# Kernel optimization log

Measured on AMD Instinct MI355X. Metric: run time of the kernel, lower is better.

## Reference

```python
import jax, jax.numpy as jnp
import numpy as np
from jax import lax

B, S, D = 1, 2048, 1280
H = 16
HD = D // H  # 80
L = 2
I = 5120
SCALE = HD ** -0.5
EPS = 1e-6
GH, GW = 64, 32  # patch grid: GH*GW == S
THETA = 10000.0


def _make_rope(dtype=jnp.float32):
    # 2D vision RoPE: half the rotary dims encode row position, half column.
    half = HD // 2  # 40
    inv_freq = 1.0 / (THETA ** (jnp.arange(0, half, 2, dtype=jnp.float32) / half))  # [20]
    hpos = jnp.repeat(jnp.arange(GH, dtype=jnp.float32), GW)  # [S]
    wpos = jnp.tile(jnp.arange(GW, dtype=jnp.float32), GH)    # [S]
    freqs = jnp.concatenate([hpos[:, None] * inv_freq, wpos[:, None] * inv_freq], axis=-1)  # [S, 40]
    emb = jnp.concatenate([freqs, freqs], axis=-1)  # [S, 80]
    return jnp.cos(emb).astype(dtype), jnp.sin(emb).astype(dtype)


def setup_inputs() -> dict:
    key = jax.random.key(0)
    ks = jax.random.split(key, 8)
    cos, sin = _make_rope()
    std = 0.02
    return {
        "hidden_states": jax.random.normal(ks[0], (B, S, D), jnp.float32),
        "cos": cos,
        "sin": sin,
        "qkv_w": jax.random.normal(ks[1], (L, D, 3 * D), jnp.float32) * std,
        "qkv_b": jnp.zeros((L, 3 * D), jnp.float32),
        "proj_w": jax.random.normal(ks[2], (L, D, D), jnp.float32) * std,
        "proj_b": jnp.zeros((L, D), jnp.float32),
        "ln1_g": jnp.ones((L, D), jnp.float32),
        "ln1_b": jnp.zeros((L, D), jnp.float32),
        "ln2_g": jnp.ones((L, D), jnp.float32),
        "ln2_b": jnp.zeros((L, D), jnp.float32),
        "fc1_w": jax.random.normal(ks[3], (L, D, I), jnp.float32) * std,
        "fc1_b": jnp.zeros((L, I), jnp.float32),
        "fc2_w": jax.random.normal(ks[4], (L, I, D), jnp.float32) * std,
        "fc2_b": jnp.zeros((L, D), jnp.float32),
    }


def _layernorm(x, g, b):
    m = jnp.mean(x, axis=-1, keepdims=True)
    v = jnp.mean(jnp.square(x - m), axis=-1, keepdims=True)
    return (x - m) * lax.rsqrt(v + EPS) * g + b


def _rotate_half(x):
    h = x.shape[-1] // 2
    return jnp.concatenate([-x[..., h:], x[..., :h]], axis=-1)


def _block(x, cos, sin, p):
    (qkv_w, qkv_b, proj_w, proj_b, g1, b1, g2, b2, f1w, f1b, f2w, f2b) = p
    # --- attention ---
    h = _layernorm(x, g1, b1)
    qkv = h @ qkv_w + qkv_b                                    # [B,S,3D]
    qkv = qkv.reshape(B, S, 3, H, HD).transpose(2, 0, 3, 1, 4)  # [3,B,H,S,hd]
    q, k, v = qkv[0], qkv[1], qkv[2]
    q = q * cos + _rotate_half(q) * sin                        # cos/sin broadcast over B,H
    k = k * cos + _rotate_half(k) * sin
    scores = jnp.einsum("bhqd,bhkd->bhqk", q, k) * SCALE       # [B,H,S,S]
    w = jax.nn.softmax(scores.astype(jnp.float32), axis=-1).astype(x.dtype)
    o = jnp.einsum("bhqk,bhkd->bhqd", w, v)
    o = o.transpose(0, 2, 1, 3).reshape(B, S, D)
    x = x + (o @ proj_w + proj_b)
    # --- MLP ---
    h = _layernorm(x, g2, b2)
    x = x + jax.nn.gelu(h @ f1w + f1b, approximate=False) @ f2w + f2b
    return x


def reference(hidden_states, cos, sin, qkv_w, qkv_b, proj_w, proj_b,
              ln1_g, ln1_b, ln2_g, ln2_b, fc1_w, fc1_b, fc2_w, fc2_b):
    params = (qkv_w, qkv_b, proj_w, proj_b, ln1_g, ln1_b,
              ln2_g, ln2_b, fc1_w, fc1_b, fc2_w, fc2_b)

    def step(x, p):
        return _block(x, cos, sin, p), None

    out, _ = lax.scan(step, hidden_states, params)
    return out
```

## Files before the change

kernel.cpp:

```cpp
#include <hip/hip_runtime.h>
#include <hip/hip_bf16.h>

using bf16 = __hip_bfloat16;
using short8 = __attribute__((ext_vector_type(8))) short;
using f32x4  = __attribute__((ext_vector_type(4))) float;

#define GLDS16(g, l) __builtin_amdgcn_global_load_lds( \
    (const __attribute__((address_space(1))) void*)(g), \
    (__attribute__((address_space(3))) void*)(l), 16, 0, 0)

constexpr int S  = 2048;
constexpr int D  = 1280;
constexpr int H  = 16;
constexpr int HD = 80;
constexpr int IM = 5120;

__global__ __launch_bounds__(256) void transpose_w(const float* __restrict__ W,
                                                   bf16* __restrict__ Wt,
                                                   int K, int N) {
  __shared__ float t[32][33];
  int tx = threadIdx.x & 31, ty = threadIdx.x >> 5;
  int n0 = blockIdx.x * 32, k0 = blockIdx.y * 32;
#pragma unroll
  for (int i = 0; i < 4; i++)
    t[ty + i * 8][tx] = W[(size_t)(k0 + ty + i * 8) * N + n0 + tx];
  __syncthreads();
#pragma unroll
  for (int i = 0; i < 4; i++)
    Wt[(size_t)(n0 + ty + i * 8) * K + k0 + tx] = __float2bfloat16(t[tx][ty + i * 8]);
}

__global__ __launch_bounds__(256) void transpose_v(const bf16* __restrict__ v,
                                                   bf16* __restrict__ vt) {
  __shared__ bf16 t[16][17];
  int tx = threadIdx.x & 15, ty = threadIdx.x >> 4;
  int s0 = blockIdx.x * 16, d0 = blockIdx.y * 16, h = blockIdx.z;
  t[ty][tx] = v[(size_t)(h * S + s0 + ty) * HD + d0 + tx];
  __syncthreads();
  vt[(size_t)(h * HD + d0 + ty) * S + s0 + tx] = t[tx][ty];
}

__global__ __launch_bounds__(256) void layernorm_k(const float* __restrict__ x,
                                                   const float* __restrict__ g,
                                                   const float* __restrict__ b,
                                                   bf16* __restrict__ h) {
  int row = blockIdx.x, tid = threadIdx.x;
  const float* xr = x + (size_t)row * D;
  float v[5], s1 = 0.f, s2 = 0.f;
#pragma unroll
  for (int i = 0; i < 5; i++) {
    v[i] = xr[tid + i * 256];
    s1 += v[i]; s2 += v[i] * v[i];
  }
#pragma unroll
  for (int o = 32; o > 0; o >>= 1) {
    s1 += __shfl_down(s1, o);
    s2 += __shfl_down(s2, o);
  }
  __shared__ float r1[4], r2[4];
  if ((tid & 63) == 0) { r1[tid >> 6] = s1; r2[tid >> 6] = s2; }
  __syncthreads();
  s1 = r1[0] + r1[1] + r1[2] + r1[3];
  s2 = r2[0] + r2[1] + r2[2] + r2[3];
  float mean = s1 * (1.f / D);
  float rstd = rsqrtf(s2 * (1.f / D) - mean * mean + 1e-6f);
  bf16* hr = h + (size_t)row * D;
#pragma unroll
  for (int i = 0; i < 5; i++) {
    int c = tid + i * 256;
    hr[c] = __float2bfloat16((v[i] - mean) * rstd * g[c] + b[c]);
  }
}

__global__ __launch_bounds__(256) void rope_k(bf16* __restrict__ q, bf16* __restrict__ k,
                                              const float* __restrict__ cs,
                                              const float* __restrict__ sn) {
  int idx = blockIdx.x * 256 + threadIdx.x;
  int p  = idx % 40;
  int t  = idx / 40;
  int s  = t & (S - 1);
  int t2 = t >> 11;
  int hh = t2 & (H - 1);
  bf16* base = ((t2 >> 4) ? k : q) + (size_t)(hh * S + s) * HD;
  float c0 = cs[s * HD + p],      s0 = sn[s * HD + p];
  float c1 = cs[s * HD + p + 40], s1 = sn[s * HD + p + 40];
  float x0 = __bfloat162float(base[p]);
  float x1 = __bfloat162float(base[p + 40]);
  base[p]      = __float2bfloat16(x0 * c0 - x1 * s0);
  base[p + 40] = __float2bfloat16(x1 * c1 + x0 * s1);
}

template <int EPI, int N, int K>
__global__ __launch_bounds__(256, 2) void gemm_bt(const bf16* __restrict__ A,
                                                  const bf16* __restrict__ Bt,
                                                  const float* __restrict__ bias,
                                                  float* __restrict__ X,
                                                  bf16* __restrict__ O) {
  __shared__ __align__(16) short As[128 * 32];
  __shared__ __align__(16) short Bs[128 * 32];
  int tid = threadIdx.x, lane = tid & 63, wid = tid >> 6;
  int l15 = lane & 15, l4 = lane >> 4;
  int wr = wid >> 1, wc = wid & 1;
  int rowBase = blockIdx.y * 128, colBase = blockIdx.x * 128;
  const bf16* Ab = A  + (size_t)rowBase * K;
  const bf16* Bb = Bt + (size_t)colBase * K;

  f32x4 acc[4][4] = {};

  for (int kt = 0; kt < K / 32; kt++) {
#pragma unroll
    for (int i = 0; i < 2; i++) {
      int cb = wid * 128 + i * 64;
      int c  = cb + lane;
      GLDS16(Ab + (c >> 2) * K + kt * 32 + (c & 3) * 8, As + cb * 8);
      GLDS16(Bb + (c >> 2) * K + kt * 32 + (c & 3) * 8, Bs + cb * 8);
    }
    __syncthreads();
    short8 af[4], bfv[4];
    const short8* Av = (const short8*)As;
    const short8* Bv = (const short8*)Bs;
#pragma unroll
    for (int i = 0; i < 4; i++) {
      af[i]  = Av[(wr * 64 + i * 16 + l15) * 4 + l4];
      bfv[i] = Bv[(wc * 64 + i * 16 + l15) * 4 + l4];
    }
#pragma unroll
    for (int m = 0; m < 4; m++)
#pragma unroll
      for (int n = 0; n < 4; n++)
        acc[m][n] = __builtin_amdgcn_mfma_f32_16x16x32_bf16(af[m], bfv[n], acc[m][n], 0, 0, 0);
    __syncthreads();
  }

#pragma unroll
  for (int m = 0; m < 4; m++) {
#pragma unroll
    for (int n = 0; n < 4; n++) {
      int col = colBase + wc * 64 + n * 16 + l15;
      float bs = bias[col];
      int row0 = rowBase + wr * 64 + m * 16 + l4 * 4;
#pragma unroll
      for (int j = 0; j < 4; j++) {
        float val = acc[m][n][j] + bs;
        int row = row0 + j;
        if (EPI == 0) {
          int which = col / D;
          int r2 = col - which * D;
          int hh = r2 / HD, d = r2 - hh * HD;
          O[(size_t)((which * H + hh) * S + row) * HD + d] = __float2bfloat16(val);
        } else if (EPI == 1) {
          X[(size_t)row * N + col] += val;
        } else {
          float gl = 0.5f * val * (1.0f + erff(val * 0.70710678118654752f));
          O[(size_t)row * N + col] = __float2bfloat16(gl);
        }
      }
    }
  }
}

__global__ __launch_bounds__(256) void flash_k(const bf16* __restrict__ q,
                                               const bf16* __restrict__ k,
                                               const bf16* __restrict__ vt,
                                               bf16* __restrict__ o) {
  __shared__ __align__(16) bf16 Qs[128 * 80];
  __shared__ __align__(16) bf16 Ks[64 * 80];
  __shared__ __align__(16) bf16 Vts[80 * 64];
  __shared__ __align__(16) bf16 Ps[128 * 72];
  const float scale = 0.11180339887498949f;
  int tid = threadIdx.x, lane = tid & 63, wid = tid >> 6;
  int l15 = lane & 15, l4 = lane >> 4;
  int hh = blockIdx.y, qb = blockIdx.x * 128;

  const bf16* qg = q + (size_t)(hh * S + qb) * HD;
#pragma unroll
  for (int i = 0; i < 5; i++) {
    int cb = i * 256 + wid * 64;
    GLDS16(qg + (size_t)(cb + lane) * 8, Qs + cb * 8);
  }

  f32x4 oacc[2][5] = {};
  float mst[2][4], lst[2][4];
#pragma unroll
  for (int m = 0; m < 2; m++)
#pragma unroll
    for (int j = 0; j < 4; j++) { mst[m][j] = -3.0e38f; lst[m][j] = 0.f; }

  const short8 zero8 = {0, 0, 0, 0, 0, 0, 0, 0};
  __syncthreads();

  for (int kt = 0; kt < S / 64; kt++) {
    const bf16* kg = k + (size_t)(hh * S + kt * 64) * HD;
    const bf16* vg = vt + (size_t)hh * HD * S + kt * 64;
#pragma unroll
    for (int i = 0; i < 2; i++) {
      int cb = i * 256 + wid * 64;
      int c  = cb + lane;
      GLDS16(kg + c * 8, Ks + cb * 8);
      int hd = c >> 3, cc = (c & 7) ^ (hd & 7);
      GLDS16(vg + hd * S + cc * 8, Vts + cb * 8);
    }
    if (wid < 2) {
      int cb = 512 + wid * 64;
      int c  = cb + lane;
      GLDS16(kg + c * 8, Ks + cb * 8);
      int hd = c >> 3, cc = (c & 7) ^ (hd & 7);
      GLDS16(vg + hd * S + cc * 8, Vts + cb * 8);
    }
    __syncthreads();

    f32x4 sacc[2][4] = {};
#pragma unroll
    for (int kf = 0; kf < 3; kf++) {
      bool act = (kf < 2) || (l4 < 2);
      short8 aq[2], bk[4];
#pragma unroll
      for (int m = 0; m < 2; m++)
        aq[m] = act ? *(const short8*)&Qs[(wid * 32 + m * 16 + l15) * 80 + (kf * 4 + l4) * 8] : zero8;
#pragma unroll
      for (int n = 0; n < 4; n++)
        bk[n] = act ? *(const short8*)&Ks[(n * 16 + l15) * 80 + (kf * 4 + l4) * 8] : zero8;
#pragma unroll
      for (int m = 0; m < 2; m++)
#pragma unroll
        for (int n = 0; n < 4; n++)
          sacc[m][n] = __builtin_amdgcn_mfma_f32_16x16x32_bf16(aq[m], bk[n], sacc[m][n], 0, 0, 0);
    }

#pragma unroll
    for (int m = 0; m < 2; m++) {
#pragma unroll
      for (int j = 0; j < 4; j++) {
        float s0 = sacc[m][0][j] * scale, s1 = sacc[m][1][j] * scale;
        float s2 = sacc[m][2][j] * scale, s3 = sacc[m][3][j] * scale;
        float mx = fmaxf(fmaxf(s0, s1), fmaxf(s2, s3));
        mx = fmaxf(mx, __shfl_xor(mx, 1));
        mx = fmaxf(mx, __shfl_xor(mx, 2));
        mx = fmaxf(mx, __shfl_xor(mx, 4));
        mx = fmaxf(mx, __shfl_xor(mx, 8));
        float newm = fmaxf(mst[m][j], mx);
        float fac = __expf(mst[m][j] - newm);
        mst[m][j] = newm;
        float p0 = __expf(s0 - newm), p1 = __expf(s1 - newm);
        float p2 = __expf(s2 - newm), p3 = __expf(s3 - newm);
        int prow = wid * 32 + m * 16 + l4 * 4 + j;
        Ps[prow * 72 +      l15] = __float2bfloat16(p0);
        Ps[prow * 72 + 16 + l15] = __float2bfloat16(p1);
        Ps[prow * 72 + 32 + l15] = __float2bfloat16(p2);
        Ps[prow * 72 + 48 + l15] = __float2bfloat16(p3);
        float ps = p0 + p1 + p2 + p3;
        ps += __shfl_xor(ps, 1);
        ps += __shfl_xor(ps, 2);
        ps += __shfl_xor(ps, 4);
        ps += __shfl_xor(ps, 8);
        lst[m][j] = lst[m][j] * fac + ps;
#pragma unroll
        for (int n5 = 0; n5 < 5; n5++) oacc[m][n5][j] *= fac;
      }
    }

#pragma unroll
    for (int kf = 0; kf < 2; kf++) {
      short8 ap[2], bv[5];
#pragma unroll
      for (int m = 0; m < 2; m++)
        ap[m] = *(const short8*)&Ps[(wid * 32 + m * 16 + l15) * 72 + (kf * 4 + l4) * 8];
#pragma unroll
      for (int n5 = 0; n5 < 5; n5++) {
        int hd = n5 * 16 + l15;
        int cc = (kf * 4 + l4) ^ (hd & 7);
        bv[n5] = *(const short8*)&Vts[hd * 64 + cc * 8];
      }
#pragma unroll
      for (int m = 0; m < 2; m++)
#pragma unroll
        for (int n5 = 0; n5 < 5; n5++)
          oacc[m][n5] = __builtin_amdgcn_mfma_f32_16x16x32_bf16(ap[m], bv[n5], oacc[m][n5], 0, 0, 0);
    }
    __syncthreads();
  }

#pragma unroll
  for (int m = 0; m < 2; m++)
#pragma unroll
    for (int n5 = 0; n5 < 5; n5++)
#pragma unroll
      for (int j = 0; j < 4; j++) {
        int row = qb + wid * 32 + m * 16 + l4 * 4 + j;
        int col = hh * HD + n5 * 16 + l15;
        o[(size_t)row * D + col] = __float2bfloat16(oacc[m][n5][j] / lst[m][j]);
      }
}

extern "C" void kernel_launch(void* const* d_in, const int* in_sizes, int n_in,
                              void* d_out, int out_size, void* d_ws, size_t ws_size,
                              hipStream_t stream) {
  const float* hidden = (const float*)d_in[0];
  const float* cosp   = (const float*)d_in[1];
  const float* sinp   = (const float*)d_in[2];
  const float* qkv_w  = (const float*)d_in[3];
  const float* qkv_b  = (const float*)d_in[4];
  const float* proj_w = (const float*)d_in[5];
  const float* proj_b = (const float*)d_in[6];
  const float* ln1_g  = (const float*)d_in[7];
  const float* ln1_b  = (const float*)d_in[8];
  const float* ln2_g  = (const float*)d_in[9];
  const float* ln2_b  = (const float*)d_in[10];
  const float* fc1_w  = (const float*)d_in[11];
  const float* fc1_b  = (const float*)d_in[12];
  const float* fc2_w  = (const float*)d_in[13];
  const float* fc2_b  = (const float*)d_in[14];
  float* x = (float*)d_out;

  char* w = (char*)d_ws;
  auto alloc = [&](size_t bytes) { void* p = (void*)w; w += bytes; return p; };
  bf16* wqkvT = (bf16*)alloc((size_t)3 * D * D * 2);
  bf16* wprojT = (bf16*)alloc((size_t)D * D * 2);
  bf16* wfc1T = (bf16*)alloc((size_t)IM * D * 2);
  bf16* wfc2T = (bf16*)alloc((size_t)D * IM * 2);
  bf16* hbuf  = (bf16*)alloc((size_t)S * D * 2);
  bf16* qkvb  = (bf16*)alloc((size_t)3 * H * S * HD * 2);
  bf16* vtbuf = (bf16*)alloc((size_t)H * HD * S * 2);
  bf16* obuf  = (bf16*)alloc((size_t)S * D * 2);
  bf16* midb  = (bf16*)alloc((size_t)S * IM * 2);
  (void)ws_size; (void)in_sizes; (void)n_in; (void)out_size;

  hipMemcpyAsync(x, hidden, (size_t)S * D * sizeof(float), hipMemcpyDeviceToDevice, stream);

  for (int l = 0; l < 2; l++) {
    transpose_w<<<dim3(3 * D / 32, D / 32), 256, 0, stream>>>(qkv_w + (size_t)l * D * 3 * D, wqkvT, D, 3 * D);
    transpose_w<<<dim3(D / 32, D / 32), 256, 0, stream>>>(proj_w + (size_t)l * D * D, wprojT, D, D);
    transpose_w<<<dim3(IM / 32, D / 32), 256, 0, stream>>>(fc1_w + (size_t)l * D * IM, wfc1T, D, IM);
    transpose_w<<<dim3(D / 32, IM / 32), 256, 0, stream>>>(fc2_w + (size_t)l * IM * D, wfc2T, IM, D);

    layernorm_k<<<S, 256, 0, stream>>>(x, ln1_g + l * D, ln1_b + l * D, hbuf);
    gemm_bt<0, 3 * D, D><<<dim3(3 * D / 128, S / 128), 256, 0, stream>>>(
        hbuf, wqkvT, qkv_b + (size_t)l * 3 * D, nullptr, qkvb);
    rope_k<<<(2 * H * S * (HD / 2)) / 256, 256, 0, stream>>>(
        qkvb, qkvb + (size_t)H * S * HD, cosp, sinp);
    transpose_v<<<dim3(S / 16, HD / 16, H), 256, 0, stream>>>(qkvb + (size_t)2 * H * S * HD, vtbuf);
    flash_k<<<dim3(S / 128, H), 256, 0, stream>>>(
        qkvb, qkvb + (size_t)H * S * HD, vtbuf, obuf);
    gemm_bt<1, D, D><<<dim3(D / 128, S / 128), 256, 0, stream>>>(
        obuf, wprojT, proj_b + l * D, x, nullptr);

    layernorm_k<<<S, 256, 0, stream>>>(x, ln2_g + l * D, ln2_b + l * D, hbuf);
    gemm_bt<2, IM, D><<<dim3(IM / 128, S / 128), 256, 0, stream>>>(
        hbuf, wfc1T, fc1_b + (size_t)l * IM, nullptr, midb);
    gemm_bt<1, D, IM><<<dim3(D / 128, S / 128), 256, 0, stream>>>(
        midb, wfc2T, fc2_b + l * D, x, nullptr);
  }
}
```

Measured before the change: 882.2 us.

## Double-buffer GEMM LDS, swizzle LDS and XCD mapping, split-K proj and fc2

The GEMM kernel now double-buffers its LDS tiles so the next K slice's global-to-LDS load overlaps the current slice's MFMAs, and it XOR-swizzles LDS chunk indices to reduce bank conflicts. Workgroup IDs are remapped so neighbouring tiles land on the same XCD for better L2 reuse. The proj and fc2 GEMMs, which have only 160 tiles, are split along K into two partial fp32 buffers that a separate reduce kernel sums with bias into the residual. This aims to raise occupancy and hide memory latency, at the cost of extra partial-sum traffic, more LDS per block, and reusing qkvb and midb as scratch space.

Result: faster. 802.3 us (-9.1%).

```diff
diff --git a/kernel.cpp b/kernel.cpp
--- a/kernel.cpp
+++ b/kernel.cpp
@@ -90,39 +90,63 @@
   base[p + 40] = __float2bfloat16(x1 * c1 + x0 * s1);
 }
 
-template <int EPI, int N, int K>
-__global__ __launch_bounds__(256, 2) void gemm_bt(const bf16* __restrict__ A,
-                                                  const bf16* __restrict__ Bt,
-                                                  const float* __restrict__ bias,
-                                                  float* __restrict__ X,
-                                                  bf16* __restrict__ O) {
-  __shared__ __align__(16) short As[128 * 32];
-  __shared__ __align__(16) short Bs[128 * 32];
+template <int EPI, int N, int K, int SPLITK>
+__global__ __launch_bounds__(256, 2) void gemm2(const bf16* __restrict__ A,
+                                                const bf16* __restrict__ Bt,
+                                                const float* __restrict__ bias,
+                                                float* __restrict__ X,
+                                                bf16* __restrict__ O,
+                                                float* __restrict__ P) {
+  __shared__ __align__(16) short As[2][128 * 32];
+  __shared__ __align__(16) short Bs[2][128 * 32];
   int tid = threadIdx.x, lane = tid & 63, wid = tid >> 6;
   int l15 = lane & 15, l4 = lane >> 4;
   int wr = wid >> 1, wc = wid & 1;
-  int rowBase = blockIdx.y * 128, colBase = blockIdx.x * 128;
-  const bf16* Ab = A  + (size_t)rowBase * K;
-  const bf16* Bb = Bt + (size_t)colBase * K;
+
+  int gx = gridDim.x;
+  int nwg = gx * (int)gridDim.y;
+  int lin = blockIdx.y * gx + blockIdx.x;
+  int q = nwg >> 3, r = nwg & 7;
+  int xcd = lin & 7, idx = lin >> 3;
+  int swz = (xcd < r ? xcd * (q + 1) : r * (q + 1) + (xcd - r) * q) + idx;
+  int bx = swz % gx, by = swz / gx;
+
+  int rowBase = by * 128, colBase = bx * 128;
+  constexpr int KS = K / SPLITK;
+  constexpr int NT = KS / 32;
+  int k0 = blockIdx.z * KS;
+  const bf16* Ab = A  + (size_t)rowBase * K + k0;
+  const bf16* Bb = Bt + (size_t)colBase * K + k0;
 
   f32x4 acc[4][4] = {};
 
-  for (int kt = 0; kt < K / 32; kt++) {
+  auto stage = [&](int buf, int kt) {
 #pragma unroll
     for (int i = 0; i < 2; i++) {
       int cb = wid * 128 + i * 64;
       int c  = cb + lane;
-      GLDS16(Ab + (c >> 2) * K + kt * 32 + (c & 3) * 8, As + cb * 8);
-      GLDS16(Bb + (c >> 2) * K + kt * 32 + (c & 3) * 8, Bs + cb * 8);
-    }
-    __syncthreads();
+      int row = c >> 2;
+      int ci  = (c & 3) ^ ((row >> 1) & 3);
+      GLDS16(Ab + (size_t)row * K + kt * 32 + ci * 8, &As[buf][cb * 8]);
+      GLDS16(Bb + (size_t)row * K + kt * 32 + ci * 8, &Bs[buf][cb * 8]);
+    }
+  };
+
+  stage(0, 0);
+  __syncthreads();
+
+  int cur = 0;
+  for (int kt = 0; kt < NT; kt++) {
+    if (kt + 1 < NT) stage(cur ^ 1, kt + 1);
     short8 af[4], bfv[4];
-    const short8* Av = (const short8*)As;
-    const short8* Bv = (const short8*)Bs;
+    const short8* Av = (const short8*)As[cur];
+    const short8* Bv = (const short8*)Bs[cur];
 #pragma unroll
     for (int i = 0; i < 4; i++) {
-      af[i]  = Av[(wr * 64 + i * 16 + l15) * 4 + l4];
-      bfv[i] = Bv[(wc * 64 + i * 16 + l15) * 4 + l4];
+      int ra = wr * 64 + i * 16 + l15;
+      int rb = wc * 64 + i * 16 + l15;
+      af[i]  = Av[ra * 4 + (l4 ^ ((ra >> 1) & 3))];
+      bfv[i] = Bv[rb * 4 + (l4 ^ ((rb >> 1) & 3))];
     }
 #pragma unroll
     for (int m = 0; m < 4; m++)
@@ -130,6 +154,7 @@
       for (int n = 0; n < 4; n++)
         acc[m][n] = __builtin_amdgcn_mfma_f32_16x16x32_bf16(af[m], bfv[n], acc[m][n], 0, 0, 0);
     __syncthreads();
+    cur ^= 1;
   }
 
 #pragma unroll
@@ -137,7 +162,7 @@
 #pragma unroll
     for (int n = 0; n < 4; n++) {
       int col = colBase + wc * 64 + n * 16 + l15;
-      float bs = bias[col];
+      float bs = (EPI == 3) ? 0.f : bias[col];
       int row0 = rowBase + wr * 64 + m * 16 + l4 * 4;
 #pragma unroll
       for (int j = 0; j < 4; j++) {
@@ -150,13 +175,31 @@
           O[(size_t)((which * H + hh) * S + row) * HD + d] = __float2bfloat16(val);
         } else if (EPI == 1) {
           X[(size_t)row * N + col] += val;
-        } else {
+        } else if (EPI == 2) {
           float gl = 0.5f * val * (1.0f + erff(val * 0.70710678118654752f));
           O[(size_t)row * N + col] = __float2bfloat16(gl);
+        } else {
+          P[(size_t)blockIdx.z * (2048 * N) + (size_t)row * N + col] = val;
         }
       }
     }
   }
+}
+
+__global__ __launch_bounds__(256) void reduce_add(const float* __restrict__ P,
+                                                  const float* __restrict__ bias,
+                                                  float* __restrict__ X) {
+  int i = blockIdx.x * 1024 + threadIdx.x * 4;
+  int col = i % D;
+  float4 p0 = *(const float4*)&P[i];
+  float4 p1 = *(const float4*)&P[(size_t)2048 * D + i];
+  float4 bv = *(const float4*)&bias[col];
+  float4 xv = *(const float4*)&X[i];
+  xv.x += p0.x + p1.x + bv.x;
+  xv.y += p0.y + p1.y + bv.y;
+  xv.z += p0.z + p1.z + bv.z;
+  xv.w += p0.w + p1.w + bv.w;
+  *(float4*)&X[i] = xv;
 }
 
 __global__ __launch_bounds__(256) void flash_k(const bf16* __restrict__ q,
@@ -314,15 +357,17 @@
 
   char* w = (char*)d_ws;
   auto alloc = [&](size_t bytes) { void* p = (void*)w; w += bytes; return p; };
-  bf16* wqkvT = (bf16*)alloc((size_t)3 * D * D * 2);
+  bf16* wqkvT  = (bf16*)alloc((size_t)3 * D * D * 2);
   bf16* wprojT = (bf16*)alloc((size_t)D * D * 2);
-  bf16* wfc1T = (bf16*)alloc((size_t)IM * D * 2);
-  bf16* wfc2T = (bf16*)alloc((size_t)D * IM * 2);
-  bf16* hbuf  = (bf16*)alloc((size_t)S * D * 2);
-  bf16* qkvb  = (bf16*)alloc((size_t)3 * H * S * HD * 2);
-  bf16* vtbuf = (bf16*)alloc((size_t)H * HD * S * 2);
-  bf16* obuf  = (bf16*)alloc((size_t)S * D * 2);
-  bf16* midb  = (bf16*)alloc((size_t)S * IM * 2);
+  bf16* wfc1T  = (bf16*)alloc((size_t)IM * D * 2);
+  bf16* wfc2T  = (bf16*)alloc((size_t)D * IM * 2);
+  bf16* hbuf   = (bf16*)alloc((size_t)S * D * 2);
+  bf16* qkvb   = (bf16*)alloc((size_t)3 * H * S * HD * 2);
+  bf16* vtbuf  = (bf16*)alloc((size_t)H * HD * S * 2);
+  bf16* obuf   = (bf16*)alloc((size_t)S * D * 2);
+  bf16* midb   = (bf16*)alloc((size_t)S * IM * 2);
+  float* Pproj = (float*)midb;
+  float* Pfc2  = (float*)qkvb;
   (void)ws_size; (void)in_sizes; (void)n_in; (void)out_size;
 
   hipMemcpyAsync(x, hidden, (size_t)S * D * sizeof(float), hipMemcpyDeviceToDevice, stream);
@@ -334,20 +379,22 @@
     transpose_w<<<dim3(D / 32, IM / 32), 256, 0, stream>>>(fc2_w + (size_t)l * IM * D, wfc2T, IM, D);
 
     layernorm_k<<<S, 256, 0, stream>>>(x, ln1_g + l * D, ln1_b + l * D, hbuf);
-    gemm_bt<0, 3 * D, D><<<dim3(3 * D / 128, S / 128), 256, 0, stream>>>(
-        hbuf, wqkvT, qkv_b + (size_t)l * 3 * D, nullptr, qkvb);
+    gemm2<0, 3 * D, D, 1><<<dim3(3 * D / 128, S / 128, 1), 256, 0, stream>>>(
+        hbuf, wqkvT, qkv_b + (size_t)l * 3 * D, nullptr, qkvb, nullptr);
     rope_k<<<(2 * H * S * (HD / 2)) / 256, 256, 0, stream>>>(
         qkvb, qkvb + (size_t)H * S * HD, cosp, sinp);
     transpose_v<<<dim3(S / 16, HD / 16, H), 256, 0, stream>>>(qkvb + (size_t)2 * H * S * HD, vtbuf);
     flash_k<<<dim3(S / 128, H), 256, 0, stream>>>(
         qkvb, qkvb + (size_t)H * S * HD, vtbuf, obuf);
-    gemm_bt<1, D, D><<<dim3(D / 128, S / 128), 256, 0, stream>>>(
-        obuf, wprojT, proj_b + l * D, x, nullptr);
+    gemm2<3, D, D, 2><<<dim3(D / 128, S / 128, 2), 256, 0, stream>>>(
+        obuf, wprojT, nullptr, nullptr, nullptr, Pproj);
+    reduce_add<<<(S * D) / 1024, 256, 0, stream>>>(Pproj, proj_b + l * D, x);
 
     layernorm_k<<<S, 256, 0, stream>>>(x, ln2_g + l * D, ln2_b + l * D, hbuf);
-    gemm_bt<2, IM, D><<<dim3(IM / 128, S / 128), 256, 0, stream>>>(
-        hbuf, wfc1T, fc1_b + (size_t)l * IM, nullptr, midb);
-    gemm_bt<1, D, IM><<<dim3(D / 128, S / 128), 256, 0, stream>>>(
-        midb, wfc2T, fc2_b + l * D, x, nullptr);
-  }
-}
+    gemm2<2, IM, D, 1><<<dim3(IM / 128, S / 128, 1), 256, 0, stream>>>(
+        hbuf, wfc1T, fc1_b + (size_t)l * IM, nullptr, midb, nullptr);
+    gemm2<3, D, IM, 2><<<dim3(D / 128, S / 128, 2), 256, 0, stream>>>(
+        midb, wfc2T, nullptr, nullptr, nullptr, Pfc2);
+    reduce_add<<<(S * D) / 1024, 256, 0, stream>>>(Pfc2, fc2_b + l * D, x);
+  }
+}
```
